# Performance work log

Hardware: AMD Instinct MI355X
Metric: run time of the kernel (lower is better)

The kernel has to match this reference:

```python
import jax, jax.numpy as jnp
import numpy as np

EPS = 1e-5
SCALE = 4


def _conv(x, w, b=None, stride=1, pad=0):
    y = jax.lax.conv_general_dilated(
        x, w, (stride, stride), ((pad, pad), (pad, pad)),
        dimension_numbers=("NCHW", "OIHW", "NCHW"))
    if b is not None:
        y = y + b[None, :, None, None]
    return y


def _bn(x, g, b, m, v):
    # inference-mode BatchNorm2d with running stats
    scale = g / jnp.sqrt(v + EPS)
    return (x - m[None, :, None, None]) * scale[None, :, None, None] + b[None, :, None, None]


def setup_inputs() -> dict:
    key = jax.random.key(0)
    ks = jax.random.split(key, 20)
    B, H, W = 2, 112, 256
    d = {}
    d["patch"] = jax.random.normal(ks[0], (B, 3, SCALE * H, SCALE * W), jnp.float32)
    d["disp"] = jax.random.normal(ks[1], (B, 1, H, W), jnp.float32)
    # encode: conv(3->256, k=s=4, no bias) + BN + ReLU + conv(256->256, k3 p1, no bias) + BN + ReLU
    d["w_enc1"] = jax.random.normal(ks[2], (256, 3, SCALE, SCALE), jnp.float32) * 0.05
    d["bn1_g"] = jax.random.uniform(ks[3], (256,), jnp.float32) + 0.5
    d["bn1_b"] = jax.random.normal(ks[4], (256,), jnp.float32) * 0.01
    d["bn1_m"] = jax.random.normal(ks[5], (256,), jnp.float32) * 0.01
    d["bn1_v"] = jax.random.uniform(ks[6], (256,), jnp.float32) + 0.5
    d["w_enc2"] = jax.random.normal(ks[7], (256, 256, 3, 3), jnp.float32) * 0.02
    d["bn2_g"] = jax.random.uniform(ks[8], (256,), jnp.float32) + 0.5
    d["bn2_b"] = jax.random.normal(ks[9], (256,), jnp.float32) * 0.01
    d["bn2_m"] = jax.random.normal(ks[10], (256,), jnp.float32) * 0.01
    d["bn2_v"] = jax.random.uniform(ks[11], (256,), jnp.float32) + 0.5
    # conv_disp_feat: conv(257->256, k3 p1) + ReLU + conv(256->512, k3 p1) + ReLU + conv(512->144, k1)
    d["w_c1"] = jax.random.normal(ks[12], (256, 257, 3, 3), jnp.float32) * 0.02
    d["b_c1"] = jax.random.normal(ks[13], (256,), jnp.float32) * 0.01
    d["w_c2"] = jax.random.normal(ks[14], (512, 256, 3, 3), jnp.float32) * 0.02
    d["b_c2"] = jax.random.normal(ks[15], (512,), jnp.float32) * 0.01
    d["w_c3"] = jax.random.normal(ks[16], (SCALE * SCALE * 9, 512, 1, 1), jnp.float32) * 0.02
    d["b_c3"] = jax.random.normal(ks[17], (SCALE * SCALE * 9,), jnp.float32) * 0.01
    return d


def reference(patch, disp, w_enc1, bn1_g, bn1_b, bn1_m, bn1_v,
              w_enc2, bn2_g, bn2_b, bn2_m, bn2_v,
              w_c1, b_c1, w_c2, b_c2, w_c3, b_c3):
    B, _, H, W = disp.shape
    # encoder
    feat = jax.nn.relu(_bn(_conv(patch, w_enc1, stride=SCALE), bn1_g, bn1_b, bn1_m, bn1_v))
    feat = jax.nn.relu(_bn(_conv(feat, w_enc2, pad=1), bn2_g, bn2_b, bn2_m, bn2_v))
    # mask prediction
    x = jnp.concatenate([disp, feat], axis=1)  # (B, 257, H, W)
    x = jax.nn.relu(_conv(x, w_c1, b_c1, pad=1))
    x = jax.nn.relu(_conv(x, w_c2, b_c2, pad=1))
    raw_mask = _conv(x, w_c3, b_c3)  # (B, 144, H, W)
    mask = raw_mask.reshape(B, 1, 9, SCALE, SCALE, H, W)
    mask = jax.nn.softmax(mask, axis=2)
    # F.unfold(disp, k=3, p=1): gather 3x3 neighborhoods, order (ky, kx)
    padd = jnp.pad(disp, ((0, 0), (0, 0), (1, 1), (1, 1)))
    neigh = jnp.stack([padd[:, :, ky:ky + H, kx:kx + W]
                       for ky in range(3) for kx in range(3)], axis=2)  # (B,1,9,H,W)
    up = (mask * neigh[:, :, :, None, None, :, :]).sum(axis=2)  # (B,1,s,s,H,W)
    up = up.transpose(0, 1, 4, 2, 5, 3).reshape(B, 1, SCALE * H, SCALE * W)
    return up
```

## Files before the change

kernel.cpp:

```cpp
#include <hip/hip_runtime.h>
#include <hip/hip_bf16.h>

constexpr int B_ = 2;
constexpr int H_ = 112;
constexpr int W_ = 256;
constexpr int HW_ = H_ * W_;
constexpr int PH_ = 448;
constexpr int PW_ = 1024;
constexpr float EPS_ = 1e-5f;

typedef __bf16 bf16x8 __attribute__((ext_vector_type(8)));
typedef float f32x4 __attribute__((ext_vector_type(4)));

__device__ __forceinline__ bf16x8 ld_bf16x8(const __hip_bfloat16* p) {
    return *reinterpret_cast<const bf16x8*>(p);
}
__device__ __forceinline__ bf16x8 zero_bf16x8() {
    union { int4 i; bf16x8 v; } u;
    u.i = make_int4(0, 0, 0, 0);
    return u.v;
}
__device__ __forceinline__ void gload_lds16(const __hip_bfloat16* g, __hip_bfloat16* lds) {
    __builtin_amdgcn_global_load_lds(
        (const __attribute__((address_space(1))) void*)g,
        (__attribute__((address_space(3))) void*)lds, 16, 0, 0);
}

__global__ void prep_w3_pack(const float* __restrict__ w, int COUT, int CSRC, int COFF,
                             const float* __restrict__ g, const float* __restrict__ vvar,
                             __hip_bfloat16* __restrict__ dst) {
    int idx = blockIdx.x * 256 + threadIdx.x;
    int CF = COUT / 16;
    int n = 9 * 8 * CF * 512;
    if (idx >= n) return;
    int j = idx & 7;
    int lane = (idx >> 3) & 63;
    int rest = idx >> 9;
    int cf = rest % CF;
    int rest2 = rest / CF;
    int ks = rest2 & 7;
    int tap = rest2 >> 3;
    int cout = cf * 16 + (lane & 15);
    int ci = ks * 32 + (lane >> 4) * 8 + j;
    float sc = g ? g[cout] * rsqrtf(vvar[cout] + EPS_) : 1.f;
    dst[idx] = __float2bfloat16(w[((size_t)cout * CSRC + ci + COFF) * 9 + tap] * sc);
}

__global__ void prep_c3_pack(const float* __restrict__ w, __hip_bfloat16* __restrict__ dst) {
    int idx = blockIdx.x * 256 + threadIdx.x;
    if (idx >= 16 * 9 * 512) return;
    int j = idx & 7;
    int lane = (idx >> 3) & 63;
    int rest = idx >> 9;
    int mf = rest % 9;
    int ks = rest / 9;
    int row = mf * 16 + (lane & 15);
    int ci = ks * 32 + (lane >> 4) * 8 + j;
    dst[idx] = __float2bfloat16(w[(size_t)row * 512 + ci]);
}

__global__ void prep_misc_kernel(const float* __restrict__ w_c1,
                                 const float* __restrict__ g, const float* __restrict__ bb,
                                 const float* __restrict__ m, const float* __restrict__ v,
                                 float* __restrict__ wd_c1, float* __restrict__ bias2) {
    int idx = blockIdx.x * 256 + threadIdx.x;
    if (idx < 256 * 9) {
        int co = idx / 9, tap = idx % 9;
        wd_c1[idx] = w_c1[(size_t)co * 257 * 9 + tap];
    } else if (idx < 256 * 9 + 256) {
        int co = idx - 256 * 9;
        float sc = g[co] * rsqrtf(v[co] + EPS_);
        bias2[co] = bb[co] - m[co] * sc;
    }
}

__global__ __launch_bounds__(256) void enc1_nhwc_kernel(
    const float* __restrict__ patch, const float* __restrict__ wgt,
    const float* __restrict__ g, const float* __restrict__ bb,
    const float* __restrict__ m, const float* __restrict__ v,
    __hip_bfloat16* __restrict__ out) {
    const int tid = threadIdx.x;
    const int px = tid & 63;
    const int wid = tid >> 6;
    const int bx = blockIdx.x;
    const int w0 = (bx & 3) * 64;
    const int h = bx >> 2;
    const int b = blockIdx.z;
    const int w = w0 + px;

    float p[3][4][4];
#pragma unroll
    for (int c = 0; c < 3; ++c)
#pragma unroll
        for (int ky = 0; ky < 4; ++ky) {
            float4 f = *reinterpret_cast<const float4*>(
                patch + (((size_t)b * 3 + c) * PH_ + 4 * h + ky) * PW_ + 4 * w);
            p[c][ky][0] = f.x; p[c][ky][1] = f.y; p[c][ky][2] = f.z; p[c][ky][3] = f.w;
        }

    __shared__ __hip_bfloat16 s[64][258];

    const int kbase = __builtin_amdgcn_readfirstlane(wid * 64);
    for (int i = 0; i < 64; ++i) {
        int k = kbase + i;
        const float* wk = wgt + (size_t)k * 48;
        float acc = 0.f;
#pragma unroll
        for (int c = 0; c < 3; ++c)
#pragma unroll
            for (int ky = 0; ky < 4; ++ky)
#pragma unroll
                for (int kx = 0; kx < 4; ++kx)
                    acc += p[c][ky][kx] * wk[(c * 4 + ky) * 4 + kx];
        float sc = g[k] * rsqrtf(v[k] + EPS_);
        float o = fmaxf(acc * sc + (bb[k] - m[k] * sc), 0.f);
        s[px][k] = __float2bfloat16(o);
    }
    __syncthreads();
    const size_t base = (((size_t)b * H_ + h) * W_ + w0) * 256;
    for (int j = tid; j < 64 * 128; j += 256) {
        int elem = j * 2;
        int pp = elem >> 8;
        int k = elem & 255;
        unsigned int val = *reinterpret_cast<const unsigned int*>(&s[pp][k]);
        *reinterpret_cast<unsigned int*>(out + base + elem) = val;
    }
}

template <int COUT, bool HAS_DISP>
__global__ __launch_bounds__(512, 4) void conv3x3_swz(
    const __hip_bfloat16* __restrict__ in,
    const __hip_bfloat16* __restrict__ wPack,
    const float* __restrict__ bias,
    const float* __restrict__ disp,
    const float* __restrict__ wd,
    __hip_bfloat16* __restrict__ out) {
    constexpr int CIN = 256;
    constexpr int CF = COUT / 16;
    const int tid = threadIdx.x;
    const int lane = tid & 63;
    const int wid = tid >> 6;
    const int wm = wid & 3;
    const int wn = wid >> 2;
    const int lr = lane & 15;
    const int lg = lane >> 4;

    int bx = blockIdx.x;
    bx = (bx & 7) * 28 + (bx >> 3);
    const int w0 = (bx & 1) * 128;
    const int h = bx >> 1;
    const int coutBase = blockIdx.y * 256;
    const int b = blockIdx.z;

    const int coutW = coutBase + wm * 64;
    const int cfW = coutW >> 4;
    const int pxW = wn * 64;

    __shared__ __hip_bfloat16 sIn[2][3][130][32];

    f32x4 acc[4][4] = {};

    const __hip_bfloat16* inb = in + (size_t)b * HW_ * CIN;
    const __hip_bfloat16* wBase = wPack + (size_t)cfW * 512 + (size_t)lane * 8;

    const int key0 = (lr >> 1) & 3;
    const int key1 = ((lr + 1) >> 1) & 3;
    const int key2 = (key0 + 1) & 3;
    const int loff0 = lr * 64 + ((lg ^ key0) << 4);
    const int loff1 = lr * 64 + ((lg ^ key1) << 4);
    const int loff2 = lr * 64 + ((lg ^ key2) << 4);

    const int key_w = (((lane >> 2) + 1) >> 1) & 3;
    const int csw = (((lane & 3) ^ key_w)) * 8;

    auto STAGE = [&](int buf, int c0) {
#pragma unroll
        for (int i = 0; i < 3; ++i) {
            const int idx = wid * 3 + i;
            const int row = idx >> 3, grp = idx & 7;
            const int y = h + row - 1;
            __hip_bfloat16* ldsb = &sIn[buf][row][1 + grp * 16][0];
            if ((unsigned)y < (unsigned)H_) {
                const __hip_bfloat16* gp = inb +
                    ((size_t)y * W_ + w0 + grp * 16 + (lane >> 2)) * CIN + c0 + csw;
                gload_lds16(gp, ldsb);
            } else {
                *reinterpret_cast<int4*>(reinterpret_cast<char*>(ldsb) + lane * 16) =
                    make_int4(0, 0, 0, 0);
            }
        }
        if (tid < 24) {
            const int row = tid >> 3, p2 = (tid >> 2) & 1, sub = tid & 3;
            const int pxl = p2 ? 129 : 0;
            const int y = h + row - 1, x = w0 + pxl - 1;
            bf16x8 v = zero_bf16x8();
            if ((unsigned)y < (unsigned)H_ && (unsigned)x < (unsigned)W_)
                v = ld_bf16x8(inb + ((size_t)y * W_ + x) * CIN + c0 + sub * 8);
            *reinterpret_cast<bf16x8*>(&sIn[buf][row][pxl][sub * 8]) = v;
        }
    };

    STAGE(0, 0);
    __syncthreads();
    int cur = 0;
    for (int ks = 0; ks < 8; ++ks) {
        if (ks < 7) STAGE(cur ^ 1, (ks + 1) * 32);
        const char* sB = reinterpret_cast<const char*>(&sIn[cur][0][0][0]) + pxW * 64;
#pragma unroll
        for (int tap = 0; tap < 9; ++tap) {
            const int ky = tap / 3, kx = tap % 3;
            const int lofk = (kx == 0) ? loff0 : (kx == 1) ? loff1 : loff2;
            bf16x8 a[4];
#pragma unroll
            for (int mf = 0; mf < 4; ++mf)
                a[mf] = ld_bf16x8(wBase + ((size_t)(tap * 8 + ks) * CF + mf) * 512);
            bf16x8 bv[4];
#pragma unroll
            for (int nf = 0; nf < 4; ++nf)
                bv[nf] = *reinterpret_cast<const bf16x8*>(
                    sB + ky * 8320 + (nf * 16 + kx) * 64 + lofk);
            __builtin_amdgcn_s_setprio(1);
#pragma unroll
            for (int nf = 0; nf < 4; ++nf)
#pragma unroll
                for (int mf = 0; mf < 4; ++mf)
                    acc[mf][nf] = __builtin_amdgcn_mfma_f32_16x16x32_bf16(
                        a[mf], bv[nf], acc[mf][nf], 0, 0, 0);
            __builtin_amdgcn_s_setprio(0);
        }
        __syncthreads();
        cur ^= 1;
    }

    const size_t rowBase = ((size_t)b * H_ + h) * W_;
#pragma unroll
    for (int nf = 0; nf < 4; ++nf) {
        const int px = w0 + pxW + nf * 16 + lr;
        float dnb[9];
        if (HAS_DISP) {
#pragma unroll
            for (int t = 0; t < 9; ++t) {
                int yy = h + t / 3 - 1, xx = px + t % 3 - 1;
                dnb[t] = ((unsigned)yy < (unsigned)H_ && (unsigned)xx < (unsigned)W_)
                             ? disp[((size_t)b * H_ + yy) * W_ + xx]
                             : 0.f;
            }
        }
#pragma unroll
        for (int mf = 0; mf < 4; ++mf) {
            alignas(8) __hip_bfloat16 ov[4];
#pragma unroll
            for (int r = 0; r < 4; ++r) {
                const int cout = coutW + mf * 16 + lg * 4 + r;
                float o = acc[mf][nf][r] + bias[cout];
                if (HAS_DISP) {
                    float s = 0.f;
#pragma unroll
                    for (int t = 0; t < 9; ++t) s += wd[cout * 9 + t] * dnb[t];
                    o += s;
                }
                ov[r] = __float2bfloat16(fmaxf(o, 0.f));
            }
            *reinterpret_cast<uint2*>(out + (rowBase + px) * COUT + coutW + mf * 16 + lg * 4) =
                *reinterpret_cast<const uint2*>(ov);
        }
    }
}

__global__ __launch_bounds__(256) void c3_fused_kernel(
    const __hip_bfloat16* __restrict__ x2,
    const __hip_bfloat16* __restrict__ wPack,
    const float* __restrict__ bias,
    const float* __restrict__ disp,
    float* __restrict__ outp) {
    const int tid = threadIdx.x;
    const int lane = tid & 63;
    const int wid = tid >> 6;
    const int lr = lane & 15;
    const int lg = lane >> 4;
    const int bx = blockIdx.x;
    const int w0 = (bx & 3) * 64;
    const int h = bx >> 2;
    const int b = blockIdx.z;
    const int pxw = w0 + wid * 16 + lr;

    f32x4 acc[9] = {};
    const __hip_bfloat16* inp = x2 + (((size_t)b * H_ + h) * W_ + pxw) * 512;
    const __hip_bfloat16* wl = wPack + (size_t)lane * 8;
#pragma unroll 4
    for (int ks = 0; ks < 16; ++ks) {
        const int c0 = ks * 32 + lg * 8;
        bf16x8 bv = ld_bf16x8(inp + c0);
#pragma unroll
        for (int mf = 0; mf < 9; ++mf) {
            bf16x8 av = ld_bf16x8(wl + ((size_t)ks * 9 + mf) * 512);
            acc[mf] = __builtin_amdgcn_mfma_f32_16x16x32_bf16(av, bv, acc[mf], 0, 0, 0);
        }
    }

    float dnb[9];
#pragma unroll
    for (int t = 0; t < 9; ++t) {
        int yy = h + t / 3 - 1, xx = pxw + t % 3 - 1;
        dnb[t] = ((unsigned)yy < (unsigned)H_ && (unsigned)xx < (unsigned)W_)
                     ? disp[((size_t)b * H_ + yy) * W_ + xx]
                     : 0.f;
    }
    float oo[4];
#pragma unroll
    for (int r = 0; r < 4; ++r) {
        const int st = lg * 4 + r;
        float sv[9], mx = -1e30f;
#pragma unroll
        for (int mf = 0; mf < 9; ++mf) {
            sv[mf] = acc[mf][r] + bias[mf * 16 + st];
            mx = fmaxf(mx, sv[mf]);
        }
        float sum = 0.f, wsum = 0.f;
#pragma unroll
        for (int mf = 0; mf < 9; ++mf) {
            float e = __expf(sv[mf] - mx);
            sum += e;
            wsum += e * dnb[mf];
        }
        oo[r] = wsum / sum;
    }
    float4 o4 = make_float4(oo[0], oo[1], oo[2], oo[3]);
    *reinterpret_cast<float4*>(outp + ((size_t)b * PH_ + 4 * h + lg) * PW_ + 4 * pxw) = o4;
}

extern "C" void kernel_launch(void* const* d_in, const int* in_sizes, int n_in,
                              void* d_out, int out_size, void* d_ws, size_t ws_size,
                              hipStream_t stream) {
    const float* patch = (const float*)d_in[0];
    const float* disp = (const float*)d_in[1];
    const float* w_enc1 = (const float*)d_in[2];
    const float* bn1_g = (const float*)d_in[3];
    const float* bn1_b = (const float*)d_in[4];
    const float* bn1_m = (const float*)d_in[5];
    const float* bn1_v = (const float*)d_in[6];
    const float* w_enc2 = (const float*)d_in[7];
    const float* bn2_g = (const float*)d_in[8];
    const float* bn2_b = (const float*)d_in[9];
    const float* bn2_m = (const float*)d_in[10];
    const float* bn2_v = (const float*)d_in[11];
    const float* w_c1 = (const float*)d_in[12];
    const float* b_c1 = (const float*)d_in[13];
    const float* w_c2 = (const float*)d_in[14];
    const float* b_c2 = (const float*)d_in[15];
    const float* w_c3 = (const float*)d_in[16];
    const float* b_c3 = (const float*)d_in[17];
    float* out = (float*)d_out;

    char* ws = (char*)d_ws;
    const size_t S1 = (size_t)B_ * HW_ * 256 * sizeof(__hip_bfloat16);
    const size_t S2 = (size_t)B_ * HW_ * 512 * sizeof(__hip_bfloat16);
    __hip_bfloat16* feat1 = (__hip_bfloat16*)ws;   ws += S1;
    __hip_bfloat16* feat2 = (__hip_bfloat16*)ws;   ws += S1;
    __hip_bfloat16* x1    = (__hip_bfloat16*)ws;   ws += S1;
    __hip_bfloat16* x2    = (__hip_bfloat16*)ws;   ws += S2;
    __hip_bfloat16* wP_enc2 = (__hip_bfloat16*)ws; ws += (size_t)9 * 256 * 256 * 2;
    __hip_bfloat16* wP_c1   = (__hip_bfloat16*)ws; ws += (size_t)9 * 256 * 256 * 2;
    __hip_bfloat16* wP_c2   = (__hip_bfloat16*)ws; ws += (size_t)9 * 512 * 256 * 2;
    __hip_bfloat16* wP_c3   = (__hip_bfloat16*)ws; ws += (size_t)16 * 9 * 512 * 2;
    float* bias2 = (float*)ws;                     ws += 256 * 4;
    float* wd_c1 = (float*)ws;                     ws += 256 * 9 * 4;

    dim3 blk(256, 1, 1);
    dim3 blk2(512, 1, 1);

    prep_w3_pack<<<dim3((9 * 256 * 256 + 255) / 256), blk, 0, stream>>>(
        w_enc2, 256, 256, 0, bn2_g, bn2_v, wP_enc2);
    prep_w3_pack<<<dim3((9 * 256 * 256 + 255) / 256), blk, 0, stream>>>(
        w_c1, 256, 257, 1, nullptr, nullptr, wP_c1);
    prep_w3_pack<<<dim3((9 * 512 * 256 + 255) / 256), blk, 0, stream>>>(
        w_c2, 512, 256, 0, nullptr, nullptr, wP_c2);
    prep_c3_pack<<<dim3((16 * 9 * 512 + 255) / 256), blk, 0, stream>>>(w_c3, wP_c3);
    prep_misc_kernel<<<dim3((256 * 9 + 256 + 255) / 256), blk, 0, stream>>>(
        w_c1, bn2_g, bn2_b, bn2_m, bn2_v, wd_c1, bias2);

    enc1_nhwc_kernel<<<dim3(H_ * 4, 1, B_), blk, 0, stream>>>(
        patch, w_enc1, bn1_g, bn1_b, bn1_m, bn1_v, feat1);
    conv3x3_swz<256, false><<<dim3(2 * H_, 1, B_), blk2, 0, stream>>>(
        feat1, wP_enc2, bias2, nullptr, nullptr, feat2);
    conv3x3_swz<256, true><<<dim3(2 * H_, 1, B_), blk2, 0, stream>>>(
        feat2, wP_c1, b_c1, disp, wd_c1, x1);
    conv3x3_swz<512, false><<<dim3(2 * H_, 2, B_), blk2, 0, stream>>>(
        x1, wP_c2, b_c2, nullptr, nullptr, x2);
    c3_fused_kernel<<<dim3(H_ * 4, 1, B_), blk, 0, stream>>>(
        x2, wP_c3, b_c3, disp, out);
}
```

Baseline: 365.7 us.

## Stage conv epilogue through LDS for coalesced stores; widen c3 tile to two pixel blocks

```diff
diff --git a/kernel.cpp b/kernel.cpp
--- a/kernel.cpp
+++ b/kernel.cpp
@@ -232,42 +232,59 @@
         cur ^= 1;
     }
 
+    __hip_bfloat16* sOut = &sIn[0][0][0][0];
     const size_t rowBase = ((size_t)b * H_ + h) * W_;
-#pragma unroll
-    for (int nf = 0; nf < 4; ++nf) {
-        const int px = w0 + pxW + nf * 16 + lr;
-        float dnb[9];
-        if (HAS_DISP) {
-#pragma unroll
-            for (int t = 0; t < 9; ++t) {
-                int yy = h + t / 3 - 1, xx = px + t % 3 - 1;
-                dnb[t] = ((unsigned)yy < (unsigned)H_ && (unsigned)xx < (unsigned)W_)
-                             ? disp[((size_t)b * H_ + yy) * W_ + xx]
-                             : 0.f;
+
+#pragma unroll 1
+    for (int r2 = 0; r2 < 2; ++r2) {
+        if (wn == r2) {
+#pragma unroll
+            for (int nf = 0; nf < 4; ++nf) {
+                const int pxl = nf * 16 + lr;
+                const int px = w0 + r2 * 64 + pxl;
+                float dnb[9];
+                if (HAS_DISP) {
+#pragma unroll
+                    for (int t = 0; t < 9; ++t) {
+                        int yy = h + t / 3 - 1, xx = px + t % 3 - 1;
+                        dnb[t] = ((unsigned)yy < (unsigned)H_ && (unsigned)xx < (unsigned)W_)
+                                     ? disp[((size_t)b * H_ + yy) * W_ + xx]
+                                     : 0.f;
+                    }
+                }
+#pragma unroll
+                for (int mf = 0; mf < 4; ++mf) {
+                    alignas(8) __hip_bfloat16 ov[4];
+#pragma unroll
+                    for (int r = 0; r < 4; ++r) {
+                        const int cout = coutW + mf * 16 + lg * 4 + r;
+                        float o = acc[mf][nf][r] + bias[cout];
+                        if (HAS_DISP) {
+                            float s = 0.f;
+#pragma unroll
+                            for (int t = 0; t < 9; ++t) s += wd[cout * 9 + t] * dnb[t];
+                            o += s;
+                        }
+                        ov[r] = __float2bfloat16(fmaxf(o, 0.f));
+                    }
+                    const int cl = wm * 64 + mf * 16 + lg * 4;
+                    *reinterpret_cast<uint2*>(&sOut[pxl * 264 + cl]) =
+                        *reinterpret_cast<const uint2*>(ov);
+                }
             }
         }
-#pragma unroll
-        for (int mf = 0; mf < 4; ++mf) {
-            alignas(8) __hip_bfloat16 ov[4];
-#pragma unroll
-            for (int r = 0; r < 4; ++r) {
-                const int cout = coutW + mf * 16 + lg * 4 + r;
-                float o = acc[mf][nf][r] + bias[cout];
-                if (HAS_DISP) {
-                    float s = 0.f;
-#pragma unroll
-                    for (int t = 0; t < 9; ++t) s += wd[cout * 9 + t] * dnb[t];
-                    o += s;
-                }
-                ov[r] = __float2bfloat16(fmaxf(o, 0.f));
-            }
-            *reinterpret_cast<uint2*>(out + (rowBase + px) * COUT + coutW + mf * 16 + lg * 4) =
-                *reinterpret_cast<const uint2*>(ov);
-        }
-    }
-}
-
-__global__ __launch_bounds__(256) void c3_fused_kernel(
+        __syncthreads();
+        for (int j = tid; j < 64 * 32; j += 512) {
+            const int pxl = j >> 5, ch = j & 31;
+            bf16x8 v = *reinterpret_cast<const bf16x8*>(&sOut[pxl * 264 + ch * 8]);
+            *reinterpret_cast<bf16x8*>(
+                out + (rowBase + w0 + r2 * 64 + pxl) * COUT + coutBase + ch * 8) = v;
+        }
+        __syncthreads();
+    }
+}
+
+__global__ __launch_bounds__(256, 2) void c3_fused_kernel(
     const __hip_bfloat16* __restrict__ x2,
     const __hip_bfloat16* __restrict__ wPack,
     const float* __restrict__ bias,
@@ -279,54 +296,60 @@
     const int lr = lane & 15;
     const int lg = lane >> 4;
     const int bx = blockIdx.x;
-    const int w0 = (bx & 3) * 64;
-    const int h = bx >> 2;
+    const int w0 = (bx & 1) * 128;
+    const int h = bx >> 1;
     const int b = blockIdx.z;
-    const int pxw = w0 + wid * 16 + lr;
-
-    f32x4 acc[9] = {};
-    const __hip_bfloat16* inp = x2 + (((size_t)b * H_ + h) * W_ + pxw) * 512;
+    const int pxbase = w0 + wid * 32 + lr;
+
+    f32x4 acc[9][2] = {};
+    const __hip_bfloat16* xbase = x2 + (((size_t)b * H_ + h) * W_ + pxbase) * 512;
     const __hip_bfloat16* wl = wPack + (size_t)lane * 8;
 #pragma unroll 4
     for (int ks = 0; ks < 16; ++ks) {
         const int c0 = ks * 32 + lg * 8;
-        bf16x8 bv = ld_bf16x8(inp + c0);
+        bf16x8 bv0 = ld_bf16x8(xbase + c0);
+        bf16x8 bv1 = ld_bf16x8(xbase + 16 * 512 + c0);
 #pragma unroll
         for (int mf = 0; mf < 9; ++mf) {
             bf16x8 av = ld_bf16x8(wl + ((size_t)ks * 9 + mf) * 512);
-            acc[mf] = __builtin_amdgcn_mfma_f32_16x16x32_bf16(av, bv, acc[mf], 0, 0, 0);
-        }
-    }
-
-    float dnb[9];
-#pragma unroll
-    for (int t = 0; t < 9; ++t) {
-        int yy = h + t / 3 - 1, xx = pxw + t % 3 - 1;
-        dnb[t] = ((unsigned)yy < (unsigned)H_ && (unsigned)xx < (unsigned)W_)
-                     ? disp[((size_t)b * H_ + yy) * W_ + xx]
-                     : 0.f;
-    }
-    float oo[4];
-#pragma unroll
-    for (int r = 0; r < 4; ++r) {
-        const int st = lg * 4 + r;
-        float sv[9], mx = -1e30f;
-#pragma unroll
-        for (int mf = 0; mf < 9; ++mf) {
-            sv[mf] = acc[mf][r] + bias[mf * 16 + st];
-            mx = fmaxf(mx, sv[mf]);
-        }
-        float sum = 0.f, wsum = 0.f;
-#pragma unroll
-        for (int mf = 0; mf < 9; ++mf) {
-            float e = __expf(sv[mf] - mx);
-            sum += e;
-            wsum += e * dnb[mf];
-        }
-        oo[r] = wsum / sum;
-    }
-    float4 o4 = make_float4(oo[0], oo[1], oo[2], oo[3]);
-    *reinterpret_cast<float4*>(outp + ((size_t)b * PH_ + 4 * h + lg) * PW_ + 4 * pxw) = o4;
+            acc[mf][0] = __builtin_amdgcn_mfma_f32_16x16x32_bf16(av, bv0, acc[mf][0], 0, 0, 0);
+            acc[mf][1] = __builtin_amdgcn_mfma_f32_16x16x32_bf16(av, bv1, acc[mf][1], 0, 0, 0);
+        }
+    }
+
+#pragma unroll
+    for (int nf = 0; nf < 2; ++nf) {
+        const int pxw = pxbase + nf * 16;
+        float dnb[9];
+#pragma unroll
+        for (int t = 0; t < 9; ++t) {
+            int yy = h + t / 3 - 1, xx = pxw + t % 3 - 1;
+            dnb[t] = ((unsigned)yy < (unsigned)H_ && (unsigned)xx < (unsigned)W_)
+                         ? disp[((size_t)b * H_ + yy) * W_ + xx]
+                         : 0.f;
+        }
+        float oo[4];
+#pragma unroll
+        for (int r = 0; r < 4; ++r) {
+            const int st = lg * 4 + r;
+            float sv[9], mx = -1e30f;
+#pragma unroll
+            for (int mf = 0; mf < 9; ++mf) {
+                sv[mf] = acc[mf][nf][r] + bias[mf * 16 + st];
+                mx = fmaxf(mx, sv[mf]);
+            }
+            float sum = 0.f, wsum = 0.f;
+#pragma unroll
+            for (int mf = 0; mf < 9; ++mf) {
+                float e = __expf(sv[mf] - mx);
+                sum += e;
+                wsum += e * dnb[mf];
+            }
+            oo[r] = wsum / sum;
+        }
+        float4 o4 = make_float4(oo[0], oo[1], oo[2], oo[3]);
+        *reinterpret_cast<float4*>(outp + ((size_t)b * PH_ + 4 * h + lg) * PW_ + 4 * pxw) = o4;
+    }
 }
 
 extern "C" void kernel_launch(void* const* d_in, const int* in_sizes, int n_in,
@@ -387,6 +410,6 @@
         feat2, wP_c1, b_c1, disp, wd_c1, x1);
     conv3x3_swz<512, false><<<dim3(2 * H_, 2, B_), blk2, 0, stream>>>(
         x1, wP_c2, b_c2, nullptr, nullptr, x2);
-    c3_fused_kernel<<<dim3(H_ * 4, 1, B_), blk, 0, stream>>>(
+    c3_fused_kernel<<<dim3(2 * H_, 1, B_), blk, 0, stream>>>(
         x2, wP_c3, b_c3, disp, out);
 }
```

After: 370.9 us. No clear change (+1.4%).
